# Performance work log

Measured on AMD Instinct MI355X. Metric: run time of the kernel, lower is better.

Reference implementation:

```python
import jax, jax.numpy as jnp
import numpy as np
import math

D = 512; NA = 128; NC = 256; NB = 128; BATCH = 4; H = 8
EA, EC, EB = 4, 6, 4
KA, KC, KB = 2, 1, 2
F = 4 * D  # expert_ff_mult * embed_dim
N_TOTAL = NA + NC + NB


def setup_inputs() -> dict:
    key = jax.random.key(0)
    ks = jax.random.split(key, 16)
    s = 0.02
    def nrm(k, shape, scale=s):
        return jax.random.normal(k, shape, dtype=jnp.float32) * scale
    return {
        'tokens_A': jax.random.normal(ks[0], (BATCH, NA, D), dtype=jnp.float32),
        'tokens_B': jax.random.normal(ks[1], (BATCH, NB, D), dtype=jnp.float32),
        'tokens_C': jax.random.normal(ks[2], (BATCH, NC, D), dtype=jnp.float32),
        'ln1_g': jnp.ones((3, D), jnp.float32), 'ln1_b': jnp.zeros((3, D), jnp.float32),
        'ln2_g': jnp.ones((3, D), jnp.float32), 'ln2_b': jnp.zeros((3, D), jnp.float32),
        'Wqkv': nrm(ks[3], (3 * D, D)), 'bqkv': jnp.zeros((3 * D,), jnp.float32),
        'Wo': nrm(ks[4], (D, D)), 'bo': jnp.zeros((D,), jnp.float32),
        'Wr_A': nrm(ks[5], (D, EA)), 'br_A': jnp.zeros((EA,), jnp.float32),
        'W1_A': nrm(ks[6], (EA, D, F)), 'b1_A': jnp.zeros((EA, F), jnp.float32),
        'W2_A': nrm(ks[7], (EA, F, D)), 'b2_A': jnp.zeros((EA, D), jnp.float32),
        'Wr_C': nrm(ks[8], (D, EC)), 'br_C': jnp.zeros((EC,), jnp.float32),
        'W1_C': nrm(ks[9], (EC, D, F)), 'b1_C': jnp.zeros((EC, F), jnp.float32),
        'W2_C': nrm(ks[10], (EC, F, D)), 'b2_C': jnp.zeros((EC, D), jnp.float32),
        'Wr_B': nrm(ks[11], (D, EB)), 'br_B': jnp.zeros((EB,), jnp.float32),
        'W1_B': nrm(ks[12], (EB, D, F)), 'b1_B': jnp.zeros((EB, F), jnp.float32),
        'W2_B': nrm(ks[13], (EB, F, D)), 'b2_B': jnp.zeros((EB, D), jnp.float32),
    }


def _ln(x, g, b, eps=1e-5):
    m = jnp.mean(x, axis=-1, keepdims=True)
    v = jnp.var(x, axis=-1, keepdims=True)
    return (x - m) * jax.lax.rsqrt(v + eps) * g + b


def _directed_mask_bias():
    # segments: 0=A, 1=C, 2=B in [A|C|B] order; query may attend upstream groups only
    seg = jnp.concatenate([jnp.zeros(NA), jnp.ones(NC), 2.0 * jnp.ones(NB)])
    allowed = seg[None, :] <= seg[:, None]  # (N, N)
    return jnp.where(allowed, 0.0, -1e9).astype(jnp.float32)


def _mha(x, Wqkv, bqkv, Wo, bo, mask_bias):
    B, N, _ = x.shape
    qkv = x @ Wqkv.T + bqkv  # (B, N, 3D)
    q, k, v = jnp.split(qkv, 3, axis=-1)
    hd = D // H
    def heads(t):
        return t.reshape(B, N, H, hd).transpose(0, 2, 1, 3)  # (B, H, N, hd)
    q, k, v = heads(q), heads(k), heads(v)
    scores = jnp.einsum('bhqd,bhkd->bhqk', q, k) / math.sqrt(hd) + mask_bias[None, None]
    attn = jax.nn.softmax(scores, axis=-1)
    o = jnp.einsum('bhqk,bhkd->bhqd', attn, v).transpose(0, 2, 1, 3).reshape(B, N, D)
    return o @ Wo.T + bo


def _moe(x, Wr, br, W1, b1, W2, b2, k):
    # top-k routed expert FFN: softmax gates -> top-k renormalized -> dense combine
    probs = jax.nn.softmax(x @ Wr + br, axis=-1)  # (B, N, E)
    vals, idx = jax.lax.top_k(probs, k)
    vals = vals / jnp.sum(vals, axis=-1, keepdims=True)
    E = Wr.shape[1]
    gate = jnp.sum(jax.nn.one_hot(idx, E, dtype=x.dtype) * vals[..., None], axis=-2)  # (B, N, E)
    h = jax.nn.gelu(jnp.einsum('bnd,edf->benf', x, W1) + b1[None, :, None, :])
    y = jnp.einsum('benf,efd->bend', h, W2) + b2[None, :, None, :]
    return jnp.einsum('bne,bend->bnd', gate, y)


def reference(tokens_A, tokens_B, tokens_C, ln1_g, ln1_b, ln2_g, ln2_b,
              Wqkv, bqkv, Wo, bo,
              Wr_A, br_A, W1_A, b1_A, W2_A, b2_A,
              Wr_C, br_C, W1_C, b1_C, W2_C, b2_C,
              Wr_B, br_B, W1_B, b1_B, W2_B, b2_B):
    # 1-2. group-local pre-attention LN, concat [A | C | B]
    x = jnp.concatenate([
        _ln(tokens_A, ln1_g[0], ln1_b[0]),
        _ln(tokens_C, ln1_g[1], ln1_b[1]),
        _ln(tokens_B, ln1_g[2], ln1_b[2]),
    ], axis=1)
    # 3-4. shared directed self-attention + per-group residual
    attn = _mha(x, Wqkv, bqkv, Wo, bo, _directed_mask_bias())
    tA = tokens_A + attn[:, :NA]
    tC = tokens_C + attn[:, NA:NA + NC]
    tB = tokens_B + attn[:, NA + NC:]
    # 5. group-local pre-expert LN
    nA = _ln(tA, ln2_g[0], ln2_b[0])
    nC = _ln(tC, ln2_g[1], ln2_b[1])
    nB = _ln(tB, ln2_g[2], ln2_b[2])
    # 6-9. route A and C first, then B; residual add per group
    tA = tA + _moe(nA, Wr_A, br_A, W1_A, b1_A, W2_A, b2_A, KA)
    tC = tC + _moe(nC, Wr_C, br_C, W1_C, b1_C, W2_C, b2_C, KC)
    tB = tB + _moe(nB, Wr_B, br_B, W1_B, b1_B, W2_B, b2_B, KB)
    return jnp.concatenate([tA, tC, tB], axis=1)  # (B, NA+NC+NB, D)
```

## Files before the change

kernel.cpp:

```cpp
#include <hip/hip_runtime.h>
#include <hip/hip_bf16.h>
#include <cstdint>

#define DEV __device__ __forceinline__

using f32x4  = __attribute__((ext_vector_type(4))) float;
using bf16x8 = __attribute__((ext_vector_type(8))) __bf16;

static constexpr int D_    = 512;
static constexpr int ROWS  = 2048;
static constexpr int F_    = 2048;
static constexpr int NEXP  = 14;
static constexpr int NENT  = 3072;

DEV unsigned short f2bf(float f) {
  unsigned int u = __builtin_bit_cast(unsigned int, f);
  unsigned int r = u + 0x7FFFu + ((u >> 16) & 1u);
  return (unsigned short)(r >> 16);
}
DEV unsigned int pack2(float a, float b) {
  return (unsigned int)f2bf(a) | ((unsigned int)f2bf(b) << 16);
}
DEV float gelu_tanh(float x) {
  float x3 = x * x * x;
  return 0.5f * x * (1.0f + tanhf(0.7978845608028654f * (x + 0.044715f * x3)));
}
DEV int prefix_base(const int* cnt, int e) {
  int base = 0;
  for (int i = 0; i < e; ++i) base += cnt[i];
  return base;
}

struct Shared128 { unsigned short As[128][72]; unsigned short Bs[64][72]; };

DEV void gemm128(const unsigned short* arow, const float* B, int ldb, int bcol0, int K,
                 f32x4 (&acc)[2][4], Shared128& sh)
{
  const int tid = threadIdx.x;
  const int lane = tid & 63, w = tid >> 6;
  const int ai = tid >> 1, ah = tid & 1;
  const int bj = tid >> 2, bq = tid & 3;
  for (int k0 = 0; k0 < K; k0 += 64) {
    __syncthreads();
    {
      const uint4* src = reinterpret_cast<const uint4*>(arow + k0 + ah * 32);
      uint4 v0 = src[0], v1 = src[1], v2 = src[2], v3 = src[3];
      uint4* dst = reinterpret_cast<uint4*>(&sh.As[ai][ah * 32]);
      dst[0] = v0; dst[1] = v1; dst[2] = v2; dst[3] = v3;
    }
    {
      const float4* src = reinterpret_cast<const float4*>(B + (size_t)(bcol0 + bj) * ldb + k0 + bq * 16);
      unsigned int pk[8];
      #pragma unroll
      for (int u = 0; u < 4; ++u) {
        float4 f = src[u];
        pk[u * 2]     = pack2(f.x, f.y);
        pk[u * 2 + 1] = pack2(f.z, f.w);
      }
      uint4* dst = reinterpret_cast<uint4*>(&sh.Bs[bj][bq * 16]);
      dst[0] = make_uint4(pk[0], pk[1], pk[2], pk[3]);
      dst[1] = make_uint4(pk[4], pk[5], pk[6], pk[7]);
    }
    __syncthreads();
    #pragma unroll
    for (int ks = 0; ks < 2; ++ks) {
      bf16x8 a[2], b[4];
      #pragma unroll
      for (int mi = 0; mi < 2; ++mi)
        a[mi] = *reinterpret_cast<const bf16x8*>(&sh.As[w * 32 + mi * 16 + (lane & 15)][ks * 32 + (lane >> 4) * 8]);
      #pragma unroll
      for (int ni = 0; ni < 4; ++ni)
        b[ni] = *reinterpret_cast<const bf16x8*>(&sh.Bs[ni * 16 + (lane & 15)][ks * 32 + (lane >> 4) * 8]);
      #pragma unroll
      for (int mi = 0; mi < 2; ++mi)
        #pragma unroll
        for (int ni = 0; ni < 4; ++ni)
          acc[mi][ni] = __builtin_amdgcn_mfma_f32_16x16x32_bf16(a[mi], b[ni], acc[mi][ni], 0, 0, 0);
    }
  }
}

DEV void gemm64x128p(const unsigned short* arow, const unsigned short* Bt,
                     f32x4 (&acc)[8], unsigned short (&As)[64][72])
{
  const int tid = threadIdx.x;
  const int lane = tid & 63, w = tid >> 6;
  const int ar = tid >> 2, aq = tid & 3;
  #pragma unroll
  for (int kt = 0; kt < 8; ++kt) {
    bf16x8 b[16];
    const unsigned short* bb = Bt + kt * 8192 + lane * 8;
    #pragma unroll
    for (int f = 0; f < 16; ++f)
      b[f] = *reinterpret_cast<const bf16x8*>(bb + f * 512);
    __syncthreads();
    {
      const uint4* srcA = reinterpret_cast<const uint4*>(arow + kt * 64 + aq * 16);
      uint4 a0 = srcA[0], a1 = srcA[1];
      uint4* dstA = reinterpret_cast<uint4*>(&As[ar][aq * 16]);
      dstA[0] = a0; dstA[1] = a1;
    }
    __syncthreads();
    bf16x8 a0 = *reinterpret_cast<const bf16x8*>(&As[w * 16 + (lane & 15)][0 * 32 + (lane >> 4) * 8]);
    bf16x8 a1 = *reinterpret_cast<const bf16x8*>(&As[w * 16 + (lane & 15)][1 * 32 + (lane >> 4) * 8]);
    #pragma unroll
    for (int ni = 0; ni < 8; ++ni)
      acc[ni] = __builtin_amdgcn_mfma_f32_16x16x32_bf16(a0, b[ni * 2 + 0], acc[ni], 0, 0, 0);
    #pragma unroll
    for (int ni = 0; ni < 8; ++ni)
      acc[ni] = __builtin_amdgcn_mfma_f32_16x16x32_bf16(a1, b[ni * 2 + 1], acc[ni], 0, 0, 0);
  }
}

__global__ __launch_bounds__(256) void k_ln(
    const float* tA, const float* tC, const float* tB,
    const float* g3, const float* b3, unsigned short* out)
{
  int r = blockIdx.x;
  int b = r >> 9, n = r & 511;
  int grp = n < 128 ? 0 : (n < 384 ? 1 : 2);
  const float* src = grp == 0 ? tA + (size_t)(b * 128 + n) * D_
                   : grp == 1 ? tC + (size_t)(b * 256 + n - 128) * D_
                              : tB + (size_t)(b * 128 + n - 384) * D_;
  int tid = threadIdx.x, lane = tid & 63, w = tid >> 6;
  float2 v = *reinterpret_cast<const float2*>(src + tid * 2);
  float s = v.x + v.y;
  float ss = v.x * v.x + v.y * v.y;
  #pragma unroll
  for (int off = 1; off < 64; off <<= 1) { s += __shfl_xor(s, off); ss += __shfl_xor(ss, off); }
  __shared__ float red[8];
  if (lane == 0) { red[w] = s; red[4 + w] = ss; }
  __syncthreads();
  float S  = red[0] + red[1] + red[2] + red[3];
  float SS = red[4] + red[5] + red[6] + red[7];
  float mean = S * (1.0f / 512.0f);
  float var  = SS * (1.0f / 512.0f) - mean * mean;
  float inv  = rsqrtf(var + 1e-5f);
  const float* gam = g3 + grp * D_;
  const float* bet = b3 + grp * D_;
  int d0 = tid * 2;
  out[(size_t)r * D_ + d0]     = f2bf((v.x - mean) * inv * gam[d0]     + bet[d0]);
  out[(size_t)r * D_ + d0 + 1] = f2bf((v.y - mean) * inv * gam[d0 + 1] + bet[d0 + 1]);
}

__global__ __launch_bounds__(256) void k_qkv(const unsigned short* x, const float* Wqkv, const float* bqkv,
                                             unsigned short* Qg, unsigned short* Kg, unsigned short* Vg)
{
  __shared__ Shared128 sh;
  int bn = blockIdx.x, bm = blockIdx.y, batch = blockIdx.z;
  int tid = threadIdx.x, lane = tid & 63, w = tid >> 6;
  const unsigned short* arow = x + (size_t)(batch * 512 + bm * 128 + (tid >> 1)) * D_;
  f32x4 acc[2][4] = {};
  gemm128(arow, Wqkv, 512, bn * 64, 512, acc, sh);
  #pragma unroll
  for (int mi = 0; mi < 2; ++mi)
  #pragma unroll
  for (int ni = 0; ni < 4; ++ni)
  #pragma unroll
  for (int j = 0; j < 4; ++j) {
    int n = bm * 128 + w * 32 + mi * 16 + ((lane >> 4) << 2) + j;
    int col = bn * 64 + ni * 16 + (lane & 15);
    float val = acc[mi][ni][j] + bqkv[col];
    int part = col >> 9;
    int o = col & 511, h = o >> 6, d = o & 63;
    unsigned short* dst = part == 0 ? Qg : (part == 1 ? Kg : Vg);
    dst[(size_t)((batch * 8 + h) * 512 + n) * 64 + d] = f2bf(val);
  }
}

__global__ __launch_bounds__(64) void k_attn(const unsigned short* Qg, const unsigned short* Kg,
                                             const unsigned short* Vg, unsigned short* attn)
{
  __shared__ unsigned short Qs[16][72], Ks[64][72], VT[64][72], Ps[16][72];
  int qt16 = blockIdx.x, h = blockIdx.y, b = blockIdx.z;
  int lane = threadIdx.x;
  const unsigned short* Qb  = Qg + (size_t)((b * 8 + h) * 512) * 64;
  const unsigned short* Kbp = Kg + (size_t)((b * 8 + h) * 512) * 64;
  const unsigned short* Vbp = Vg + (size_t)((b * 8 + h) * 512) * 64;
  int q0 = qt16 * 16;
  {
    int row = lane >> 2, q4 = lane & 3;
    const uint4* src = reinterpret_cast<const uint4*>(Qb + (size_t)(q0 + row) * 64 + q4 * 16);
    uint4* dst = reinterpret_cast<uint4*>(&Qs[row][q4 * 16]);
    dst[0] = src[0]; dst[1] = src[1];
  }
  int nkt = qt16 < 8 ? 2 : (qt16 < 24 ? 6 : 8);
  float mrun[4] = { -1e30f, -1e30f, -1e30f, -1e30f };
  float lrun[4] = {};
  f32x4 o[4] = {};
  for (int kt = 0; kt < nkt; ++kt) {
    #pragma unroll
    for (int it = 0; it < 4; ++it) {
      int row = it * 16 + (lane >> 2), q4 = lane & 3;
      const uint4* ksrc = reinterpret_cast<const uint4*>(Kbp + (size_t)(kt * 64 + row) * 64 + q4 * 16);
      uint4* kdst = reinterpret_cast<uint4*>(&Ks[row][q4 * 16]);
      kdst[0] = ksrc[0]; kdst[1] = ksrc[1];
      union { uint4 u; unsigned short s[8]; } vv0, vv1;
      const uint4* vsrc = reinterpret_cast<const uint4*>(Vbp + (size_t)(kt * 64 + row) * 64 + q4 * 16);
      vv0.u = vsrc[0]; vv1.u = vsrc[1];
      #pragma unroll
      for (int jj = 0; jj < 8; ++jj) {
        VT[q4 * 16 + jj][row]     = vv0.s[jj];
        VT[q4 * 16 + 8 + jj][row] = vv1.s[jj];
      }
    }
    f32x4 s[4] = {};
    #pragma unroll
    for (int ks = 0; ks < 2; ++ks) {
      bf16x8 aq = *reinterpret_cast<const bf16x8*>(&Qs[lane & 15][ks * 32 + (lane >> 4) * 8]);
      #pragma unroll
      for (int cc = 0; cc < 4; ++cc) {
        bf16x8 bk = *reinterpret_cast<const bf16x8*>(&Ks[cc * 16 + (lane & 15)][ks * 32 + (lane >> 4) * 8]);
        s[cc] = __builtin_amdgcn_mfma_f32_16x16x32_bf16(aq, bk, s[cc], 0, 0, 0);
      }
    }
    #pragma unroll
    for (int rr = 0; rr < 4; ++rr) {
      float s0 = s[0][rr] * 0.125f, s1 = s[1][rr] * 0.125f;
      float s2 = s[2][rr] * 0.125f, s3 = s[3][rr] * 0.125f;
      float mx = fmaxf(fmaxf(s0, s1), fmaxf(s2, s3));
      #pragma unroll
      for (int off = 1; off < 16; off <<= 1) mx = fmaxf(mx, __shfl_xor(mx, off));
      float mn = fmaxf(mrun[rr], mx);
      float al = expf(mrun[rr] - mn);
      mrun[rr] = mn;
      float p0 = expf(s0 - mn), p1 = expf(s1 - mn), p2 = expf(s2 - mn), p3 = expf(s3 - mn);
      float ps = p0 + p1 + p2 + p3;
      #pragma unroll
      for (int off = 1; off < 16; off <<= 1) ps += __shfl_xor(ps, off);
      lrun[rr] = lrun[rr] * al + ps;
      #pragma unroll
      for (int n4 = 0; n4 < 4; ++n4) o[n4][rr] *= al;
      int prow = ((lane >> 4) << 2) + rr;
      Ps[prow][0 * 16 + (lane & 15)] = f2bf(p0);
      Ps[prow][1 * 16 + (lane & 15)] = f2bf(p1);
      Ps[prow][2 * 16 + (lane & 15)] = f2bf(p2);
      Ps[prow][3 * 16 + (lane & 15)] = f2bf(p3);
    }
    #pragma unroll
    for (int ks = 0; ks < 2; ++ks) {
      bf16x8 ap = *reinterpret_cast<const bf16x8*>(&Ps[lane & 15][ks * 32 + (lane >> 4) * 8]);
      #pragma unroll
      for (int n4 = 0; n4 < 4; ++n4) {
        bf16x8 bv = *reinterpret_cast<const bf16x8*>(&VT[n4 * 16 + (lane & 15)][ks * 32 + (lane >> 4) * 8]);
        o[n4] = __builtin_amdgcn_mfma_f32_16x16x32_bf16(ap, bv, o[n4], 0, 0, 0);
      }
    }
  }
  #pragma unroll
  for (int n4 = 0; n4 < 4; ++n4)
  #pragma unroll
  for (int rr = 0; rr < 4; ++rr) {
    int qrow = q0 + ((lane >> 4) << 2) + rr;
    int col = h * 64 + n4 * 16 + (lane & 15);
    float val = o[n4][rr] / lrun[rr];
    attn[(size_t)(b * 512 + qrow) * 512 + col] = f2bf(val);
  }
}

__global__ __launch_bounds__(256) void k_wo(const unsigned short* attn, const float* Wo, const float* bo,
                                            const float* tokA, const float* tokC, const float* tokB,
                                            float* out)
{
  __shared__ Shared128 sh;
  int bn = blockIdx.x, bm = blockIdx.y;
  int tid = threadIdx.x, lane = tid & 63, w = tid >> 6;
  const unsigned short* arow = attn + (size_t)(bm * 128 + (tid >> 1)) * D_;
  f32x4 acc[2][4] = {};
  gemm128(arow, Wo, 512, bn * 64, 512, acc, sh);
  #pragma unroll
  for (int mi = 0; mi < 2; ++mi)
  #pragma unroll
  for (int ni = 0; ni < 4; ++ni)
  #pragma unroll
  for (int j = 0; j < 4; ++j) {
    int row = bm * 128 + w * 32 + mi * 16 + ((lane >> 4) << 2) + j;
    int col = bn * 64 + ni * 16 + (lane & 15);
    float val = acc[mi][ni][j] + bo[col];
    int b = row >> 9, n = row & 511;
    float res;
    if (n < 128)      res = tokA[(size_t)(b * 128 + n) * D_ + col];
    else if (n < 384) res = tokC[(size_t)(b * 256 + n - 128) * D_ + col];
    else              res = tokB[(size_t)(b * 128 + n - 384) * D_ + col];
    out[(size_t)row * D_ + col] = res + val;
  }
}

__global__ __launch_bounds__(256) void k_router(const float* t,
    const float* ln2g, const float* ln2b,
    const float* WrA, const float* brA, const float* WrC, const float* brC,
    const float* WrB, const float* brB,
    int* cnt, int* tokexp, float* tokgate, unsigned short* nrm)
{
  int w = threadIdx.x >> 6, lane = threadIdx.x & 63;
  int r = blockIdx.x * 4 + w;
  int n = r & 511;
  int grp = n < 128 ? 0 : (n < 384 ? 1 : 2);
  int E = grp == 1 ? 6 : 4;
  int topk = grp == 1 ? 1 : 2;
  int egbase = grp == 0 ? 0 : (grp == 1 ? 4 : 10);
  const float* Wr = grp == 0 ? WrA : (grp == 1 ? WrC : WrB);
  const float* br = grp == 0 ? brA : (grp == 1 ? brC : brB);
  const float* tr = t + (size_t)r * D_;
  float xv[8];
  float s = 0.0f, ss = 0.0f;
  #pragma unroll
  for (int it = 0; it < 8; ++it) {
    float v = tr[it * 64 + lane];
    xv[it] = v; s += v; ss += v * v;
  }
  #pragma unroll
  for (int off = 1; off < 64; off <<= 1) { s += __shfl_xor(s, off); ss += __shfl_xor(ss, off); }
  float mean = s * (1.0f / 512.0f);
  float var  = ss * (1.0f / 512.0f) - mean * mean;
  float inv  = rsqrtf(var + 1e-5f);
  const float* gam = ln2g + grp * D_;
  const float* bet = ln2b + grp * D_;
  float acc[6] = {};
  #pragma unroll
  for (int it = 0; it < 8; ++it) {
    int d = it * 64 + lane;
    float nv = (xv[it] - mean) * inv * gam[d] + bet[d];
    nrm[(size_t)r * D_ + d] = f2bf(nv);
    #pragma unroll
    for (int e = 0; e < 6; ++e) if (e < E) acc[e] += nv * Wr[d * E + e];
  }
  #pragma unroll
  for (int e = 0; e < 6; ++e)
    #pragma unroll
    for (int off = 1; off < 64; off <<= 1) acc[e] += __shfl_xor(acc[e], off);
  if (lane == 0) {
    float p[6];
    float mx = -1e30f;
    #pragma unroll
    for (int e = 0; e < 6; ++e) if (e < E) { p[e] = acc[e] + br[e]; mx = fmaxf(mx, p[e]); }
    float sum = 0.0f;
    #pragma unroll
    for (int e = 0; e < 6; ++e) if (e < E) { p[e] = expf(p[e] - mx); sum += p[e]; }
    #pragma unroll
    for (int e = 0; e < 6; ++e) if (e < E) p[e] /= sum;
    int i1 = 0; float v1 = p[0];
    #pragma unroll
    for (int e = 1; e < 6; ++e) if (e < E && p[e] > v1) { v1 = p[e]; i1 = e; }
    if (topk == 1) {
      tokexp[r * 2]     = egbase + i1; tokgate[r * 2]     = 1.0f;
      tokexp[r * 2 + 1] = -1;          tokgate[r * 2 + 1] = 0.0f;
      atomicAdd(&cnt[egbase + i1], 1);
    } else {
      int i2 = -1; float v2 = -1e30f;
      #pragma unroll
      for (int e = 0; e < 6; ++e) if (e < E && e != i1 && p[e] > v2) { v2 = p[e]; i2 = e; }
      float tot = v1 + v2;
      tokexp[r * 2]     = egbase + i1; tokgate[r * 2]     = v1 / tot;
      tokexp[r * 2 + 1] = egbase + i2; tokgate[r * 2 + 1] = v2 / tot;
      atomicAdd(&cnt[egbase + i1], 1);
      atomicAdd(&cnt[egbase + i2], 1);
    }
  }
}

__global__ __launch_bounds__(256) void k_scatter(const int* tokexp, const float* tokgate,
                                                 const int* cnt, int* cursor, int* list, float* gate)
{
  int r = blockIdx.x * 256 + threadIdx.x;
  #pragma unroll
  for (int j = 0; j < 2; ++j) {
    int e = tokexp[r * 2 + j];
    if (e >= 0) {
      int base = prefix_base(cnt, e);
      int s = atomicAdd(&cursor[e], 1);
      list[base + s] = r;
      gate[base + s] = tokgate[r * 2 + j];
    }
  }
}

__global__ __launch_bounds__(256) void k_pack(
    const float* w1A, const float* w1C, const float* w1B,
    const float* w2A, const float* w2C, const float* w2B,
    unsigned short* W1P, unsigned short* W2P)
{
  int bx = blockIdx.x, z = blockIdx.y;
  const float* src;
  unsigned short* dstbase;
  int ld, ntile, ktile, KT;
  if (z < 14) {
    int e = z;
    src = e < 4 ? w1A + (size_t)e * D_ * F_ : e < 10 ? w1C + (size_t)(e - 4) * D_ * F_ : w1B + (size_t)(e - 10) * D_ * F_;
    dstbase = W1P + (size_t)e * F_ * D_;
    ld = F_; KT = 8;
    ntile = bx >> 3; ktile = bx & 7;
  } else {
    int e = z - 14;
    src = e < 4 ? w2A + (size_t)e * F_ * D_ : e < 10 ? w2C + (size_t)(e - 4) * F_ * D_ : w2B + (size_t)(e - 10) * F_ * D_;
    dstbase = W2P + (size_t)e * D_ * F_;
    ld = D_; KT = 32;
    ntile = bx >> 5; ktile = bx & 31;
  }
  int k0 = ktile * 64, n0 = ntile * 128;
  __shared__ unsigned short sh[64][138];
  int t = threadIdx.x;
  {
    int r = t >> 2, q = t & 3;
    const float4* sp = reinterpret_cast<const float4*>(src + (size_t)(k0 + r) * ld + n0 + q * 32);
    unsigned int* shw = reinterpret_cast<unsigned int*>(&sh[r][q * 32]);
    #pragma unroll
    for (int u = 0; u < 8; ++u) {
      float4 v = sp[u];
      shw[u * 2]     = pack2(v.x, v.y);
      shw[u * 2 + 1] = pack2(v.z, v.w);
    }
  }
  __syncthreads();
  size_t tbase = (size_t)(ntile * KT + ktile) * 8192;
  #pragma unroll
  for (int i = 0; i < 4; ++i) {
    int p = t + 256 * i;
    int f = p >> 6, l = p & 63;
    int ks = f & 1, ni = f >> 1;
    int nl = ni * 16 + (l & 15);
    int kl = ks * 32 + (l >> 4) * 8;
    unsigned short tmp[8];
    #pragma unroll
    for (int j = 0; j < 8; ++j) tmp[j] = sh[kl + j][nl];
    *reinterpret_cast<uint4*>(dstbase + tbase + (size_t)p * 8) = *reinterpret_cast<const uint4*>(tmp);
  }
}

__global__ __launch_bounds__(256) void k_moe1(const unsigned short* nrm, const unsigned short* W1P,
    const float* b1A, const float* b1C, const float* b1B,
    const int* cnt, const int* list, unsigned short* H)
{
  int ft = blockIdx.x, tt = blockIdx.y, e = blockIdx.z;
  int c = cnt[e];
  if (tt * 64 >= c) return;
  __shared__ unsigned short As[64][72];
  const float* b1 = e < 4 ? b1A + (size_t)e * F_ : e < 10 ? b1C + (size_t)(e - 4) * F_ : b1B + (size_t)(e - 10) * F_;
  const unsigned short* Bt = W1P + (size_t)e * F_ * D_ + (size_t)(ft * 8) * 8192;
  int base = prefix_base(cnt, e);
  int tid = threadIdx.x, lane = tid & 63, w = tid >> 6;
  int ig = tt * 64 + (tid >> 2);
  int tok = list[base + (ig < c ? ig : c - 1)];
  const unsigned short* arow = nrm + (size_t)tok * D_;
  f32x4 acc[8] = {};
  gemm64x128p(arow, Bt, acc, As);
  #pragma unroll
  for (int ni = 0; ni < 8; ++ni)
  #pragma unroll
  for (int j = 0; j < 4; ++j) {
    int rl = w * 16 + ((lane >> 4) << 2) + j;
    int sg = tt * 64 + rl;
    if (sg < c) {
      int col = ft * 128 + ni * 16 + (lane & 15);
      float val = acc[ni][j] + b1[col];
      H[(size_t)(base + sg) * F_ + col] = f2bf(gelu_tanh(val));
    }
  }
}

__global__ __launch_bounds__(256) void k_moe2(const unsigned short* H, const unsigned short* W2P,
    const float* b2A, const float* b2C, const float* b2B,
    const int* cnt, const int* list, const float* gate, float* out)
{
  int dt = blockIdx.x, tt = blockIdx.y >> 2, kc = blockIdx.y & 3, e = blockIdx.z;
  int c = cnt[e];
  if (tt * 64 >= c) return;
  __shared__ unsigned short As[64][72];
  const float* b2 = e < 4 ? b2A + (size_t)e * D_ : e < 10 ? b2C + (size_t)(e - 4) * D_ : b2B + (size_t)(e - 10) * D_;
  const unsigned short* Bt = W2P + (size_t)e * D_ * F_ + (size_t)(dt * 32 + kc * 8) * 8192;
  int base = prefix_base(cnt, e);
  int tid = threadIdx.x, lane = tid & 63, w = tid >> 6;
  int ig = tt * 64 + (tid >> 2);
  const unsigned short* arow = H + (size_t)(base + (ig < c ? ig : c - 1)) * F_ + kc * 512;
  f32x4 acc[8] = {};
  gemm64x128p(arow, Bt, acc, As);
  #pragma unroll
  for (int ni = 0; ni < 8; ++ni)
  #pragma unroll
  for (int j = 0; j < 4; ++j) {
    int rl = w * 16 + ((lane >> 4) << 2) + j;
    int sg = tt * 64 + rl;
    if (sg < c) {
      int col = dt * 128 + ni * 16 + (lane & 15);
      float val = acc[ni][j] + (kc == 0 ? b2[col] : 0.0f);
      int tok = list[base + sg];
      atomicAdd(&out[(size_t)tok * D_ + col], gate[base + sg] * val);
    }
  }
}

extern "C" void kernel_launch(void* const* d_in, const int* in_sizes, int n_in,
                              void* d_out, int out_size, void* d_ws, size_t ws_size,
                              hipStream_t stream)
{
  const float* tokA = (const float*)d_in[0];
  const float* tokB = (const float*)d_in[1];
  const float* tokC = (const float*)d_in[2];
  const float* ln1g = (const float*)d_in[3];
  const float* ln1b = (const float*)d_in[4];
  const float* ln2g = (const float*)d_in[5];
  const float* ln2b = (const float*)d_in[6];
  const float* Wqkv = (const float*)d_in[7];
  const float* bqkv = (const float*)d_in[8];
  const float* Wo   = (const float*)d_in[9];
  const float* bo   = (const float*)d_in[10];
  const float* WrA  = (const float*)d_in[11];
  const float* brA  = (const float*)d_in[12];
  const float* W1A  = (const float*)d_in[13];
  const float* b1A  = (const float*)d_in[14];
  const float* W2A  = (const float*)d_in[15];
  const float* b2A  = (const float*)d_in[16];
  const float* WrC  = (const float*)d_in[17];
  const float* brC  = (const float*)d_in[18];
  const float* W1C  = (const float*)d_in[19];
  const float* b1C  = (const float*)d_in[20];
  const float* W2C  = (const float*)d_in[21];
  const float* b2C  = (const float*)d_in[22];
  const float* WrB  = (const float*)d_in[23];
  const float* brB  = (const float*)d_in[24];
  const float* W1B  = (const float*)d_in[25];
  const float* b1B  = (const float*)d_in[26];
  const float* W2B  = (const float*)d_in[27];
  const float* b2B  = (const float*)d_in[28];
  float* out = (float*)d_out;

  char* ws = (char*)d_ws;
  const size_t MB = 1024 * 1024;
  const size_t WSTRIDE = (size_t)NEXP * F_ * D_ * 2;
  unsigned short* xb   = (unsigned short*)(ws);
  unsigned short* nrm  = xb;
  unsigned short* Qg   = (unsigned short*)(ws + 2 * MB);
  unsigned short* Kg   = (unsigned short*)(ws + 4 * MB);
  unsigned short* Vg   = (unsigned short*)(ws + 6 * MB);
  unsigned short* attn = (unsigned short*)(ws + 8 * MB);
  unsigned short* W1P  = (unsigned short*)(ws + 16 * MB);
  unsigned short* W2P  = (unsigned short*)(ws + 16 * MB + WSTRIDE);
  unsigned short* H    = (unsigned short*)(ws + 16 * MB + 2 * WSTRIDE);
  char* small = ws + 16 * MB + 2 * WSTRIDE + (size_t)NENT * F_ * 2;
  int*   cnt     = (int*)(small);
  int*   cursor  = (int*)(small + 64);
  int*   tokexp  = (int*)(small + 256);
  float* tokgate = (float*)(small + 256 + ROWS * 2 * 4);
  int*   list    = (int*)(small + 256 + ROWS * 4 * 4);
  float* gate    = (float*)(small + 256 + ROWS * 4 * 4 + NENT * 4);

  hipMemsetAsync(cnt, 0, 128, stream);
  k_ln<<<ROWS, 256, 0, stream>>>(tokA, tokC, tokB, ln1g, ln1b, xb);
  k_qkv<<<dim3(24, 4, 4), 256, 0, stream>>>(xb, Wqkv, bqkv, Qg, Kg, Vg);
  k_attn<<<dim3(32, 8, 4), 64, 0, stream>>>(Qg, Kg, Vg, attn);
  k_wo<<<dim3(8, 16), 256, 0, stream>>>(attn, Wo, bo, tokA, tokC, tokB, out);
  k_router<<<512, 256, 0, stream>>>(out, ln2g, ln2b, WrA, brA, WrC, brC, WrB, brB,
                                    cnt, tokexp, tokgate, nrm);
  k_scatter<<<8, 256, 0, stream>>>(tokexp, tokgate, cnt, cursor, list, gate);
  k_pack<<<dim3(128, 28), 256, 0, stream>>>(W1A, W1C, W1B, W2A, W2C, W2B, W1P, W2P);
  k_moe1<<<dim3(16, 16, 14), 256, 0, stream>>>(nrm, W1P, b1A, b1C, b1B, cnt, list, H);
  k_moe2<<<dim3(4, 64, 14), 256, 0, stream>>>(H, W2P, b2A, b2C, b2B, cnt, list, gate, out);
}
```

Measured before the change: 246.0 us.

## Merge weight packing into QKV launch and stage MoE B tiles through LDS

```diff
diff --git a/kernel.cpp b/kernel.cpp
--- a/kernel.cpp
+++ b/kernel.cpp
@@ -80,35 +80,39 @@
   }
 }
 
-DEV void gemm64x128p(const unsigned short* arow, const unsigned short* Bt,
-                     f32x4 (&acc)[8], unsigned short (&As)[64][72])
+struct SharedMoE { unsigned short As[64][72]; unsigned short Bs[8192]; };
+
+DEV void gemm64x128L(const unsigned short* arow, const unsigned short* Bt,
+                     f32x4 (&acc)[8], SharedMoE& sh)
 {
   const int tid = threadIdx.x;
   const int lane = tid & 63, w = tid >> 6;
   const int ar = tid >> 2, aq = tid & 3;
   #pragma unroll
   for (int kt = 0; kt < 8; ++kt) {
-    bf16x8 b[16];
-    const unsigned short* bb = Bt + kt * 8192 + lane * 8;
-    #pragma unroll
-    for (int f = 0; f < 16; ++f)
-      b[f] = *reinterpret_cast<const bf16x8*>(bb + f * 512);
     __syncthreads();
     {
       const uint4* srcA = reinterpret_cast<const uint4*>(arow + kt * 64 + aq * 16);
       uint4 a0 = srcA[0], a1 = srcA[1];
-      uint4* dstA = reinterpret_cast<uint4*>(&As[ar][aq * 16]);
+      uint4* dstA = reinterpret_cast<uint4*>(&sh.As[ar][aq * 16]);
       dstA[0] = a0; dstA[1] = a1;
     }
+    {
+      const uint4* srcB = reinterpret_cast<const uint4*>(Bt + kt * 8192 + tid * 32);
+      uint4 b0 = srcB[0], b1 = srcB[1], b2 = srcB[2], b3 = srcB[3];
+      uint4* dstB = reinterpret_cast<uint4*>(&sh.Bs[tid * 32]);
+      dstB[0] = b0; dstB[1] = b1; dstB[2] = b2; dstB[3] = b3;
+    }
     __syncthreads();
-    bf16x8 a0 = *reinterpret_cast<const bf16x8*>(&As[w * 16 + (lane & 15)][0 * 32 + (lane >> 4) * 8]);
-    bf16x8 a1 = *reinterpret_cast<const bf16x8*>(&As[w * 16 + (lane & 15)][1 * 32 + (lane >> 4) * 8]);
-    #pragma unroll
-    for (int ni = 0; ni < 8; ++ni)
-      acc[ni] = __builtin_amdgcn_mfma_f32_16x16x32_bf16(a0, b[ni * 2 + 0], acc[ni], 0, 0, 0);
-    #pragma unroll
-    for (int ni = 0; ni < 8; ++ni)
-      acc[ni] = __builtin_amdgcn_mfma_f32_16x16x32_bf16(a1, b[ni * 2 + 1], acc[ni], 0, 0, 0);
+    bf16x8 a0 = *reinterpret_cast<const bf16x8*>(&sh.As[w * 16 + (lane & 15)][0 * 32 + (lane >> 4) * 8]);
+    bf16x8 a1 = *reinterpret_cast<const bf16x8*>(&sh.As[w * 16 + (lane & 15)][1 * 32 + (lane >> 4) * 8]);
+    #pragma unroll
+    for (int ni = 0; ni < 8; ++ni) {
+      bf16x8 b0 = *reinterpret_cast<const bf16x8*>(&sh.Bs[(ni * 2 + 0) * 512 + lane * 8]);
+      bf16x8 b1 = *reinterpret_cast<const bf16x8*>(&sh.Bs[(ni * 2 + 1) * 512 + lane * 8]);
+      acc[ni] = __builtin_amdgcn_mfma_f32_16x16x32_bf16(a0, b0, acc[ni], 0, 0, 0);
+      acc[ni] = __builtin_amdgcn_mfma_f32_16x16x32_bf16(a1, b1, acc[ni], 0, 0, 0);
+    }
   }
 }
 
@@ -143,28 +147,83 @@
   out[(size_t)r * D_ + d0 + 1] = f2bf((v.y - mean) * inv * gam[d0 + 1] + bet[d0 + 1]);
 }
 
-__global__ __launch_bounds__(256) void k_qkv(const unsigned short* x, const float* Wqkv, const float* bqkv,
-                                             unsigned short* Qg, unsigned short* Kg, unsigned short* Vg)
-{
-  __shared__ Shared128 sh;
-  int bn = blockIdx.x, bm = blockIdx.y, batch = blockIdx.z;
-  int tid = threadIdx.x, lane = tid & 63, w = tid >> 6;
-  const unsigned short* arow = x + (size_t)(batch * 512 + bm * 128 + (tid >> 1)) * D_;
-  f32x4 acc[2][4] = {};
-  gemm128(arow, Wqkv, 512, bn * 64, 512, acc, sh);
-  #pragma unroll
-  for (int mi = 0; mi < 2; ++mi)
-  #pragma unroll
-  for (int ni = 0; ni < 4; ++ni)
-  #pragma unroll
-  for (int j = 0; j < 4; ++j) {
-    int n = bm * 128 + w * 32 + mi * 16 + ((lane >> 4) << 2) + j;
-    int col = bn * 64 + ni * 16 + (lane & 15);
-    float val = acc[mi][ni][j] + bqkv[col];
-    int part = col >> 9;
-    int o = col & 511, h = o >> 6, d = o & 63;
-    unsigned short* dst = part == 0 ? Qg : (part == 1 ? Kg : Vg);
-    dst[(size_t)((batch * 8 + h) * 512 + n) * 64 + d] = f2bf(val);
+__global__ __launch_bounds__(256) void k_qkv_pack(
+    const unsigned short* x, const float* Wqkv, const float* bqkv,
+    unsigned short* Qg, unsigned short* Kg, unsigned short* Vg,
+    const float* w1A, const float* w1C, const float* w1B,
+    const float* w2A, const float* w2C, const float* w2B,
+    unsigned short* W1P, unsigned short* W2P)
+{
+  __shared__ __align__(16) char smem[sizeof(Shared128)];
+  int bid = blockIdx.x;
+  int tid = threadIdx.x;
+  if (bid < 384) {
+    Shared128& sh = *reinterpret_cast<Shared128*>(smem);
+    int bn = bid % 24, bm = (bid / 24) % 4, batch = bid / 96;
+    int lane = tid & 63, w = tid >> 6;
+    const unsigned short* arow = x + (size_t)(batch * 512 + bm * 128 + (tid >> 1)) * D_;
+    f32x4 acc[2][4] = {};
+    gemm128(arow, Wqkv, 512, bn * 64, 512, acc, sh);
+    #pragma unroll
+    for (int mi = 0; mi < 2; ++mi)
+    #pragma unroll
+    for (int ni = 0; ni < 4; ++ni)
+    #pragma unroll
+    for (int j = 0; j < 4; ++j) {
+      int n = bm * 128 + w * 32 + mi * 16 + ((lane >> 4) << 2) + j;
+      int col = bn * 64 + ni * 16 + (lane & 15);
+      float val = acc[mi][ni][j] + bqkv[col];
+      int part = col >> 9;
+      int o = col & 511, h = o >> 6, d = o & 63;
+      unsigned short* dst = part == 0 ? Qg : (part == 1 ? Kg : Vg);
+      dst[(size_t)((batch * 8 + h) * 512 + n) * 64 + d] = f2bf(val);
+    }
+  } else {
+    int pbid = bid - 384;
+    int bx = pbid & 127, z = pbid >> 7;
+    const float* src;
+    unsigned short* dstbase;
+    int ld, ntile, ktile, KT;
+    if (z < 14) {
+      int e = z;
+      src = e < 4 ? w1A + (size_t)e * D_ * F_ : e < 10 ? w1C + (size_t)(e - 4) * D_ * F_ : w1B + (size_t)(e - 10) * D_ * F_;
+      dstbase = W1P + (size_t)e * F_ * D_;
+      ld = F_; KT = 8;
+      ntile = bx >> 3; ktile = bx & 7;
+    } else {
+      int e = z - 14;
+      src = e < 4 ? w2A + (size_t)e * F_ * D_ : e < 10 ? w2C + (size_t)(e - 4) * F_ * D_ : w2B + (size_t)(e - 10) * F_ * D_;
+      dstbase = W2P + (size_t)e * D_ * F_;
+      ld = D_; KT = 32;
+      ntile = bx >> 5; ktile = bx & 31;
+    }
+    int k0 = ktile * 64, n0 = ntile * 128;
+    auto sh = reinterpret_cast<unsigned short (*)[138]>(smem);
+    {
+      int r = tid >> 2, q = tid & 3;
+      const float4* sp = reinterpret_cast<const float4*>(src + (size_t)(k0 + r) * ld + n0 + q * 32);
+      unsigned int* shw = reinterpret_cast<unsigned int*>(&sh[r][q * 32]);
+      #pragma unroll
+      for (int u = 0; u < 8; ++u) {
+        float4 v = sp[u];
+        shw[u * 2]     = pack2(v.x, v.y);
+        shw[u * 2 + 1] = pack2(v.z, v.w);
+      }
+    }
+    __syncthreads();
+    size_t tbase = (size_t)(ntile * KT + ktile) * 8192;
+    #pragma unroll
+    for (int i = 0; i < 4; ++i) {
+      int p = tid + 256 * i;
+      int f = p >> 6, l = p & 63;
+      int ks = f & 1, ni = f >> 1;
+      int nl = ni * 16 + (l & 15);
+      int kl = ks * 32 + (l >> 4) * 8;
+      unsigned short tmp[8];
+      #pragma unroll
+      for (int j = 0; j < 8; ++j) tmp[j] = sh[kl + j][nl];
+      *reinterpret_cast<uint4*>(dstbase + tbase + (size_t)p * 8) = *reinterpret_cast<const uint4*>(tmp);
+    }
   }
 }
 
@@ -375,58 +434,6 @@
   }
 }
 
-__global__ __launch_bounds__(256) void k_pack(
-    const float* w1A, const float* w1C, const float* w1B,
-    const float* w2A, const float* w2C, const float* w2B,
-    unsigned short* W1P, unsigned short* W2P)
-{
-  int bx = blockIdx.x, z = blockIdx.y;
-  const float* src;
-  unsigned short* dstbase;
-  int ld, ntile, ktile, KT;
-  if (z < 14) {
-    int e = z;
-    src = e < 4 ? w1A + (size_t)e * D_ * F_ : e < 10 ? w1C + (size_t)(e - 4) * D_ * F_ : w1B + (size_t)(e - 10) * D_ * F_;
-    dstbase = W1P + (size_t)e * F_ * D_;
-    ld = F_; KT = 8;
-    ntile = bx >> 3; ktile = bx & 7;
-  } else {
-    int e = z - 14;
-    src = e < 4 ? w2A + (size_t)e * F_ * D_ : e < 10 ? w2C + (size_t)(e - 4) * F_ * D_ : w2B + (size_t)(e - 10) * F_ * D_;
-    dstbase = W2P + (size_t)e * D_ * F_;
-    ld = D_; KT = 32;
-    ntile = bx >> 5; ktile = bx & 31;
-  }
-  int k0 = ktile * 64, n0 = ntile * 128;
-  __shared__ unsigned short sh[64][138];
-  int t = threadIdx.x;
-  {
-    int r = t >> 2, q = t & 3;
-    const float4* sp = reinterpret_cast<const float4*>(src + (size_t)(k0 + r) * ld + n0 + q * 32);
-    unsigned int* shw = reinterpret_cast<unsigned int*>(&sh[r][q * 32]);
-    #pragma unroll
-    for (int u = 0; u < 8; ++u) {
-      float4 v = sp[u];
-      shw[u * 2]     = pack2(v.x, v.y);
-      shw[u * 2 + 1] = pack2(v.z, v.w);
-    }
-  }
-  __syncthreads();
-  size_t tbase = (size_t)(ntile * KT + ktile) * 8192;
-  #pragma unroll
-  for (int i = 0; i < 4; ++i) {
-    int p = t + 256 * i;
-    int f = p >> 6, l = p & 63;
-    int ks = f & 1, ni = f >> 1;
-    int nl = ni * 16 + (l & 15);
-    int kl = ks * 32 + (l >> 4) * 8;
-    unsigned short tmp[8];
-    #pragma unroll
-    for (int j = 0; j < 8; ++j) tmp[j] = sh[kl + j][nl];
-    *reinterpret_cast<uint4*>(dstbase + tbase + (size_t)p * 8) = *reinterpret_cast<const uint4*>(tmp);
-  }
-}
-
 __global__ __launch_bounds__(256) void k_moe1(const unsigned short* nrm, const unsigned short* W1P,
     const float* b1A, const float* b1C, const float* b1B,
     const int* cnt, const int* list, unsigned short* H)
@@ -434,7 +441,7 @@
   int ft = blockIdx.x, tt = blockIdx.y, e = blockIdx.z;
   int c = cnt[e];
   if (tt * 64 >= c) return;
-  __shared__ unsigned short As[64][72];
+  __shared__ SharedMoE sh;
   const float* b1 = e < 4 ? b1A + (size_t)e * F_ : e < 10 ? b1C + (size_t)(e - 4) * F_ : b1B + (size_t)(e - 10) * F_;
   const unsigned short* Bt = W1P + (size_t)e * F_ * D_ + (size_t)(ft * 8) * 8192;
   int base = prefix_base(cnt, e);
@@ -443,7 +450,7 @@
   int tok = list[base + (ig < c ? ig : c - 1)];
   const unsigned short* arow = nrm + (size_t)tok * D_;
   f32x4 acc[8] = {};
-  gemm64x128p(arow, Bt, acc, As);
+  gemm64x128L(arow, Bt, acc, sh);
   #pragma unroll
   for (int ni = 0; ni < 8; ++ni)
   #pragma unroll
@@ -465,7 +472,7 @@
   int dt = blockIdx.x, tt = blockIdx.y >> 2, kc = blockIdx.y & 3, e = blockIdx.z;
   int c = cnt[e];
   if (tt * 64 >= c) return;
-  __shared__ unsigned short As[64][72];
+  __shared__ SharedMoE sh;
   const float* b2 = e < 4 ? b2A + (size_t)e * D_ : e < 10 ? b2C + (size_t)(e - 4) * D_ : b2B + (size_t)(e - 10) * D_;
   const unsigned short* Bt = W2P + (size_t)e * D_ * F_ + (size_t)(dt * 32 + kc * 8) * 8192;
   int base = prefix_base(cnt, e);
@@ -473,7 +480,7 @@
   int ig = tt * 64 + (tid >> 2);
   const unsigned short* arow = H + (size_t)(base + (ig < c ? ig : c - 1)) * F_ + kc * 512;
   f32x4 acc[8] = {};
-  gemm64x128p(arow, Bt, acc, As);
+  gemm64x128L(arow, Bt, acc, sh);
   #pragma unroll
   for (int ni = 0; ni < 8; ++ni)
   #pragma unroll
@@ -546,13 +553,13 @@
 
   hipMemsetAsync(cnt, 0, 128, stream);
   k_ln<<<ROWS, 256, 0, stream>>>(tokA, tokC, tokB, ln1g, ln1b, xb);
-  k_qkv<<<dim3(24, 4, 4), 256, 0, stream>>>(xb, Wqkv, bqkv, Qg, Kg, Vg);
+  k_qkv_pack<<<3968, 256, 0, stream>>>(xb, Wqkv, bqkv, Qg, Kg, Vg,
+                                       W1A, W1C, W1B, W2A, W2C, W2B, W1P, W2P);
   k_attn<<<dim3(32, 8, 4), 64, 0, stream>>>(Qg, Kg, Vg, attn);
   k_wo<<<dim3(8, 16), 256, 0, stream>>>(attn, Wo, bo, tokA, tokC, tokB, out);
   k_router<<<512, 256, 0, stream>>>(out, ln2g, ln2b, WrA, brA, WrC, brC, WrB, brB,
                                     cnt, tokexp, tokgate, nrm);
   k_scatter<<<8, 256, 0, stream>>>(tokexp, tokgate, cnt, cursor, list, gate);
-  k_pack<<<dim3(128, 28), 256, 0, stream>>>(W1A, W1C, W1B, W2A, W2C, W2B, W1P, W2P);
   k_moe1<<<dim3(16, 16, 14), 256, 0, stream>>>(nrm, W1P, b1A, b1C, b1B, cnt, list, H);
   k_moe2<<<dim3(4, 64, 14), 256, 0, stream>>>(H, W2P, b2A, b2C, b2B, cnt, list, gate, out);
 }
```

New measurement: 223.9 us. 9.0% less time.
